# Optimization experiments

Hardware: AMD Instinct MI355X
Metric: run time of the kernel (lower is better)

## Reference

```python
import jax, jax.numpy as jnp
import numpy as np
import math

B, S, D, H = 2, 2048, 1024, 16
HD = D // H  # head_dim = 64
ROPE_BASE = 100000
EPS = 1e-09


def _linear_init(key, in_f, out_f):
    std = min(1.0, math.sqrt(out_f / in_f)) / math.sqrt(in_f)
    return jax.random.normal(key, (in_f, out_f)) * std


def setup_inputs() -> dict:
    key = jax.random.key(0)
    ks = jax.random.split(key, 7)
    Q = jax.random.normal(ks[0], (B, S, D), dtype=jnp.float32)
    K = jax.random.normal(ks[1], (B, S, D), dtype=jnp.float32)
    V = jax.random.normal(ks[2], (B, S, D), dtype=jnp.float32)
    mask = jnp.tril(jnp.ones((S, S), dtype=bool))  # causal
    Wq = _linear_init(ks[3], D, D)
    Wk = _linear_init(ks[4], D, D)
    Wv = _linear_init(ks[5], D, D)
    Wo = _linear_init(ks[6], D, D)
    return {"Q": Q, "K": K, "V": V, "mask": mask,
            "Wq": Wq, "Wk": Wk, "Wv": Wv, "Wo": Wo}


def _rope_tables(seq_len, d):
    positions = jnp.arange(0, seq_len)
    freqs = ROPE_BASE ** (jnp.arange(0, d, 2) / d)
    gamma = positions[:, None] * (1.0 / freqs)[None, :]  # [t, d/2]
    return jnp.cos(gamma).astype(jnp.bfloat16), jnp.sin(gamma).astype(jnp.bfloat16)


def _apply_rope(x, cos, sin):
    # x: [..., t, d]; cos/sin: [t, d/2]
    d = x.shape[-1]
    x1, x2 = x[..., : d // 2], x[..., d // 2:]
    y1 = x1 * cos + x2 * sin
    y2 = -x1 * sin + x2 * cos
    return jnp.concatenate([y1, y2], axis=-1)


def _rms_norm(x):
    rms = jnp.sqrt(jnp.mean(jnp.square(x), axis=-1, keepdims=True) + EPS)
    return x / rms


def reference(Q, K, V, mask, Wq, Wk, Wv, Wo):
    cos, sin = _rope_tables(S, HD)
    q = jnp.dot(Q, Wq)
    k = jnp.dot(K, Wk)
    v = jnp.dot(V, Wv)
    # [B, S, D] -> [B, H, S, HD]
    split = lambda t: t.reshape(*t.shape[:-1], H, HD).swapaxes(-3, -2)
    q, k, v = split(q), split(k), split(v)
    q = _rms_norm(_apply_rope(q, cos, sin))
    k = _rms_norm(_apply_rope(k, cos, sin))
    logits = jnp.einsum('bhqd,bhkd->bhqk', q, k) / jnp.sqrt(jnp.float32(HD))
    logits = jnp.where(mask[None, None, :, :], logits, -1000000000.0)
    attn = jax.nn.softmax(logits, axis=-1)
    vals = jnp.einsum('bhqk,bhkd->bhqd', attn, v)
    # [B, H, S, HD] -> [B, S, D]
    vals = vals.swapaxes(-3, -2).reshape(B, S, D)
    return jnp.dot(vals, Wo)
```

## Files before the change

kernel.cpp:

```cpp
#include <hip/hip_runtime.h>
#include <hip/hip_bf16.h>
#include <stdint.h>

typedef __hip_bfloat16 bf16;
typedef __attribute__((ext_vector_type(8))) short short8;
typedef __attribute__((ext_vector_type(4))) short short4v;
typedef __attribute__((ext_vector_type(4))) float float4v;

static constexpr int nB = 2, nS = 2048, nD = 1024, nH = 16, nHD = 64;
static constexpr int nBS = nB * nS;

#define AS_GLOBAL __attribute__((address_space(1)))
#define AS_LDS    __attribute__((address_space(3)))

union Frag16B { short8 v; uint4 u4; uint2 u2[2]; };

__device__ __forceinline__ void gload_lds16(const void* g, void* l) {
  __builtin_amdgcn_global_load_lds((AS_GLOBAL uint32_t*)(g), (AS_LDS uint32_t*)(l), 16, 0, 0);
}

__device__ __forceinline__ float fast_exp2(float x) {
#if __has_builtin(__builtin_amdgcn_exp2f)
  return __builtin_amdgcn_exp2f(x);
#else
  float r; asm volatile("v_exp_f32 %0, %1" : "=v"(r) : "v"(x)); return r;
#endif
}

__device__ __forceinline__ void lds_barrier() {
  asm volatile("s_waitcnt lgkmcnt(0)\ns_barrier" ::: "memory");
}

__device__ __forceinline__ void lgkm_wait() {
  asm volatile("s_waitcnt lgkmcnt(0)" ::: "memory");
}

__global__ __launch_bounds__(256) void prep_kernel(
    const float* __restrict__ Qin, const float* __restrict__ Kin, const float* __restrict__ Vin,
    const float* __restrict__ Wq, const float* __restrict__ Wk,
    const float* __restrict__ Wv, const float* __restrict__ Wo,
    bf16* __restrict__ Qbf, bf16* __restrict__ Kbf, bf16* __restrict__ Vbf,
    bf16* __restrict__ WqT, bf16* __restrict__ WkT, bf16* __restrict__ WvT, bf16* __restrict__ WoT,
    bf16* __restrict__ cos_t, bf16* __restrict__ sin_t) {
  __shared__ float tile[64][65];
  int bx = blockIdx.x, t = threadIdx.x;
  if (bx < 3072) {
    int tz = bx >> 10, blk = bx & 1023;
    const float* src = tz == 0 ? Qin : tz == 1 ? Kin : Vin;
    bf16* dst = tz == 0 ? Qbf : tz == 1 ? Kbf : Vbf;
#pragma unroll
    for (int i = 0; i < 4; ++i) {
      int idx = blk * 1024 + i * 256 + t;
      float4 v = ((const float4*)src)[idx];
      union { bf16 b[4]; uint2 u; } tmp;
      tmp.b[0] = __float2bfloat16(v.x);
      tmp.b[1] = __float2bfloat16(v.y);
      tmp.b[2] = __float2bfloat16(v.z);
      tmp.b[3] = __float2bfloat16(v.w);
      ((uint2*)dst)[idx] = tmp.u;
    }
  } else if (bx < 4096) {
    int idx = bx - 3072;
    int z = idx >> 8;
    const float* W = z == 0 ? Wq : z == 1 ? Wk : z == 2 ? Wv : Wo;
    bf16* T = z == 0 ? WqT : z == 1 ? WkT : z == 2 ? WvT : WoT;
    int tk = (idx & 15) * 64, tn = ((idx >> 4) & 15) * 64;
    int c = t & 63, r0 = t >> 6;
#pragma unroll
    for (int i = 0; i < 16; ++i) {
      int r = i * 4 + r0;
      tile[r][c] = W[(size_t)(tk + r) * nD + tn + c];
    }
    __syncthreads();
#pragma unroll
    for (int i = 0; i < 16; ++i) {
      int r = i * 4 + r0;
      T[(size_t)(tn + r) * nD + tk + c] = __float2bfloat16(tile[c][r]);
    }
  } else {
    int base = (bx - 4096) * 1024 + t * 4;
#pragma unroll
    for (int i = 0; i < 4; ++i) {
      int e = base + i;
      int s = e >> 5, j = e & 31;
      float inv_freq = powf(100000.0f, -(float)(2 * j) / 64.0f);
      float g = (float)s * inv_freq;
      cos_t[e] = __float2bfloat16(cosf(g));
      sin_t[e] = __float2bfloat16(sinf(g));
    }
  }
}

__global__ __launch_bounds__(256, 3) void gemm_qkv_kernel(
    const bf16* __restrict__ A0, const bf16* __restrict__ A1, const bf16* __restrict__ A2,
    const bf16* __restrict__ Bt0, const bf16* __restrict__ Bt1, const bf16* __restrict__ Bt2,
    bf16* __restrict__ q_h, bf16* __restrict__ k_h, bf16* __restrict__ vt_h,
    const bf16* __restrict__ cos_t, const bf16* __restrict__ sin_t) {
  const int bid = blockIdx.x;
  const int swz = (bid & 7) * 96 + (bid >> 3);
  const int z = swz >> 8;
  const int rem = swz & 255;
  const int n0 = (rem >> 5) * 128;
  const int m0 = (rem & 31) * 128;

  const bf16* __restrict__ A  = z == 0 ? A0 : (z == 1 ? A1 : A2);
  const bf16* __restrict__ Bt = z == 0 ? Bt0 : (z == 1 ? Bt1 : Bt2);

  __shared__ bf16 As[2 * 128 * 32];
  __shared__ bf16 Bs[2 * 128 * 32];

  const int t = threadIdx.x;
  const int lane = t & 63;
  const int wid = t >> 6;
  const int quad = lane >> 4;
  const int l16 = lane & 15;
  const int wm = wid >> 1;
  const int wn = wid & 1;

  const int sc    = (t & 7) ^ ((t >> 3) & 7);
  const int sml   = 2 * (t >> 3) + (sc >> 2);
  const int skoff = (sc & 3) * 8;
  const int swave = wid * 512;

  const int R0a = wm * 32 + (l16 >> 1);
  const int R0b = wn * 32 + (l16 >> 1);
  const int cpar = (l16 & 1) * 4;
  const int abase = R0a * 64 + (((cpar + quad) ^ (R0a & 7)) * 8);
  const int bbase = R0b * 64 + (((cpar + quad) ^ (R0b & 7)) * 8);

#define STAGE_A(KT, BUF) do { \
    const bf16* ag_ = A + (size_t)(m0 + sml) * nD + (KT) * 32 + skoff; \
    gload_lds16(ag_, As + (BUF) + swave); \
    gload_lds16(ag_ + (size_t)64 * nD, As + (BUF) + 2048 + swave); \
  } while (0)
#define STAGE_B(KT, BUF) do { \
    const bf16* bg_ = Bt + (size_t)(n0 + sml) * nD + (KT) * 32 + skoff; \
    gload_lds16(bg_, Bs + (BUF) + swave); \
    gload_lds16(bg_ + (size_t)64 * nD, Bs + (BUF) + 2048 + swave); \
  } while (0)

  float4v acc[4][4] = {};

  STAGE_A(0, 0);
  STAGE_B(0, 0);
  STAGE_A(1, 4096);
  asm volatile("s_waitcnt vmcnt(2)" ::: "memory");
  __builtin_amdgcn_s_barrier();

#pragma unroll 2
  for (int T = 0; T < 32; ++T) {
    const int cu = (T & 1) * 4096;
    const int nx = cu ^ 4096;

    if (T < 31) STAGE_B(T + 1, nx);
    Frag16B fa[4], fb[4];
#pragma unroll
    for (int mi = 0; mi < 4; ++mi) fa[mi].u4 = *(const uint4*)&As[cu + abase + mi * 512];
#pragma unroll
    for (int ni = 0; ni < 4; ++ni) fb[ni].u4 = *(const uint4*)&Bs[cu + bbase + ni * 512];
    __builtin_amdgcn_s_setprio(1);
#pragma unroll
    for (int mi = 0; mi < 2; ++mi)
#pragma unroll
      for (int ni = 0; ni < 4; ++ni)
        acc[mi][ni] = __builtin_amdgcn_mfma_f32_16x16x32_bf16(fa[mi].v, fb[ni].v, acc[mi][ni], 0, 0, 0);
    __builtin_amdgcn_s_setprio(0);
    __builtin_amdgcn_s_barrier();

    asm volatile("s_waitcnt lgkmcnt(0)" ::: "memory");
    __builtin_amdgcn_s_setprio(1);
#pragma unroll
    for (int ni = 0; ni < 4; ++ni)
      acc[2][ni] = __builtin_amdgcn_mfma_f32_16x16x32_bf16(fa[2].v, fb[ni].v, acc[2][ni], 0, 0, 0);
    __builtin_amdgcn_s_setprio(0);
    __builtin_amdgcn_s_barrier();

    if (T < 30) STAGE_A(T + 2, cu);
    __builtin_amdgcn_s_setprio(1);
#pragma unroll
    for (int ni = 0; ni < 4; ++ni)
      acc[3][ni] = __builtin_amdgcn_mfma_f32_16x16x32_bf16(fa[3].v, fb[ni].v, acc[3][ni], 0, 0, 0);
    __builtin_amdgcn_s_setprio(0);
    if (T < 30) { asm volatile("s_waitcnt vmcnt(2)" ::: "memory"); }
    else        { asm volatile("s_waitcnt vmcnt(0)" ::: "memory"); }
    __builtin_amdgcn_s_barrier();
  }
#undef STAGE_A
#undef STAGE_B

  const int col0 = n0 + wn * 64;
  if (z <= 1) {
    bf16* dst = z ? k_h : q_h;
#pragma unroll
    for (int mi = 0; mi < 4; ++mi)
#pragma unroll
      for (int r = 0; r < 4; ++r) {
        int row = m0 + wm * 64 + mi * 16 + quad * 4 + r;
        int s = row & (nS - 1);
        float x0 = acc[mi][0][r], x1 = acc[mi][1][r], x2 = acc[mi][2][r], x3 = acc[mi][3][r];
        float y[4];
#pragma unroll
        for (int p = 0; p < 2; ++p) {
          int d = p * 16 + l16;
          float c = __bfloat162float(cos_t[s * 32 + d]);
          float sn = __bfloat162float(sin_t[s * 32 + d]);
          float xa = p ? x1 : x0, xb = p ? x3 : x2;
          y[p] = xa * c + xb * sn;
          y[p + 2] = xb * c - xa * sn;
        }
        float ss = y[0] * y[0] + y[1] * y[1] + y[2] * y[2] + y[3] * y[3];
#pragma unroll
        for (int m = 1; m <= 8; m <<= 1) ss += __shfl_xor(ss, m, 64);
        float inv = 1.0f / sqrtf(ss * (1.0f / 64.0f) + 1e-9f);
#pragma unroll
        for (int ni = 0; ni < 4; ++ni)
          dst[(size_t)row * nD + col0 + ni * 16 + l16] = __float2bfloat16(y[ni] * inv);
      }
  } else {
#pragma unroll
    for (int mi = 0; mi < 4; ++mi)
#pragma unroll
      for (int r = 0; r < 4; ++r) {
        int row = m0 + wm * 64 + mi * 16 + quad * 4 + r;
        int b = row >> 11, s = row & (nS - 1);
#pragma unroll
        for (int ni = 0; ni < 4; ++ni) {
          int col = col0 + ni * 16 + l16;
          int h = col >> 6, d = col & 63;
          vt_h[((size_t)((b * nH + h) * 64 + d)) * nS + s] = __float2bfloat16(acc[mi][ni][r]);
        }
      }
  }
}

__global__ __launch_bounds__(256) void gemm_out_kernel(
    const bf16* __restrict__ A, const bf16* __restrict__ Bt, float* __restrict__ C) {
  __shared__ bf16 As[64 * 64];
  __shared__ bf16 Bs[128 * 64];
  const int t = threadIdx.x;
  const int lane = t & 63;
  const int wid = t >> 6;
  const int quad = lane >> 4;
  const int l16 = lane & 15;
  const int wm = wid >> 1;
  const int wn = wid & 1;
  const int m0 = blockIdx.x * 64;
  const int n0 = blockIdx.y * 128;
  const int K = nD;
  const int rloc = lane >> 3, cl = lane & 7;
  const int cg = cl ^ rloc;

  float4v acc[2][4] = {};
  for (int kt = 0; kt < K; kt += 64) {
    __syncthreads();
#pragma unroll
    for (int p = 0; p < 2; ++p) {
      int rowbase = (p * 4 + wid) * 8;
      gload_lds16(A + (size_t)(m0 + rowbase + rloc) * K + kt + cg * 8, As + (size_t)rowbase * 64);
    }
#pragma unroll
    for (int p = 0; p < 4; ++p) {
      int rowbase = (p * 4 + wid) * 8;
      gload_lds16(Bt + (size_t)(n0 + rowbase + rloc) * K + kt + cg * 8, Bs + (size_t)rowbase * 64);
    }
    __syncthreads();

#pragma unroll
    for (int ks = 0; ks < 2; ++ks) {
      Frag16B a[2], b[4];
#pragma unroll
      for (int mi = 0; mi < 2; ++mi) {
        int row = wm * 32 + mi * 16 + l16;
        int ch = (ks * 4 + quad) ^ (row & 7);
        a[mi].u4 = *(const uint4*)&As[row * 64 + ch * 8];
      }
#pragma unroll
      for (int ni = 0; ni < 4; ++ni) {
        int row = wn * 64 + ni * 16 + l16;
        int ch = (ks * 4 + quad) ^ (row & 7);
        b[ni].u4 = *(const uint4*)&Bs[row * 64 + ch * 8];
      }
#pragma unroll
      for (int mi = 0; mi < 2; ++mi)
#pragma unroll
        for (int ni = 0; ni < 4; ++ni)
          acc[mi][ni] = __builtin_amdgcn_mfma_f32_16x16x32_bf16(a[mi].v, b[ni].v, acc[mi][ni], 0, 0, 0);
    }
  }
#pragma unroll
  for (int mi = 0; mi < 2; ++mi)
#pragma unroll
    for (int ni = 0; ni < 4; ++ni)
#pragma unroll
      for (int r = 0; r < 4; ++r) {
        int row = m0 + wm * 32 + mi * 16 + quad * 4 + r;
        int col = n0 + wn * 64 + ni * 16 + l16;
        C[(size_t)row * nD + col] = acc[mi][ni][r];
      }
}

static constexpr float SC = 0.18033688011112042f;

__global__ __launch_bounds__(512, 4) void attn_kernel(const bf16* __restrict__ q_h,
                                                      const bf16* __restrict__ k_h,
                                                      const bf16* __restrict__ vt_h,
                                                      bf16* __restrict__ vals) {
  __shared__ bf16 lds_buf[4 * 8192];

  const int t = threadIdx.x;
  const int lane = t & 63, wid = t >> 6, quad = lane >> 4, l16 = lane & 15;
  const int id = blockIdx.x;
  const int xcd = id & 7;
  const int j = id >> 3;
  const int jj = j & 31;
  const int bh = xcd * 4 + (jj & 3);
  const int u = jj >> 2;
  const int qt = (j < 32) ? (15 - u) : u;
  const int b = bh >> 4, h = bh & 15;

  const bf16* Kbase = k_h + ((size_t)b * nS) * nD + h * 64;
  const bf16* Vbase = vt_h + (size_t)bh * 64 * nS;

  const int rl = lane >> 3;
  const int cg8 = ((lane & 7) ^ rl) * 8;
  const int r7 = l16 & 7;

  bf16* const scratch = lds_buf + wid * 1152;

  const int q0w = qt * 128 + wid * 16;

  Frag16B qf[2];
  {
    const bf16* qp = q_h + ((size_t)(b * nS + q0w + l16)) * nD + h * 64;
    qf[0].u4 = *(const uint4*)(qp + quad * 8);
    qf[1].u4 = *(const uint4*)(qp + 32 + quad * 8);
  }

#define STAGE_KV(KT) do { \
    const int bo_ = ((KT) & 1) * 8192; \
    const bf16* kg_ = Kbase + (size_t)((KT) * 128 + wid * 16 + rl) * nD + cg8; \
    gload_lds16(kg_, lds_buf + bo_ + wid * 1024); \
    gload_lds16(kg_ + (size_t)8 * nD, lds_buf + bo_ + wid * 1024 + 512); \
    const bf16* vg_ = Vbase + (size_t)(wid * 8 + rl) * nS + (KT) * 128 + cg8; \
    gload_lds16(vg_, lds_buf + 16384 + bo_ + wid * 512); \
    gload_lds16(vg_ + 64, lds_buf + 16384 + bo_ + 4096 + wid * 512); \
  } while (0)

#define QKH(Kb, HB, ST) do { \
    _Pragma("unroll") \
    for (int kt4 = 0; kt4 < 4; ++kt4) { \
      int row = (HB) * 64 + kt4 * 16 + l16; \
      Frag16B k0_, k1_; \
      k0_.u4 = *(const uint4*)&(Kb)[row * 64 + ((quad ^ r7) * 8)]; \
      k1_.u4 = *(const uint4*)&(Kb)[row * 64 + (((quad + 4) ^ r7) * 8)]; \
      float4v zz_ = {}; \
      zz_ = __builtin_amdgcn_mfma_f32_16x16x32_bf16(k0_.v, qf[0].v, zz_, 0, 0, 0); \
      (ST)[kt4] = __builtin_amdgcn_mfma_f32_16x16x32_bf16(k1_.v, qf[1].v, zz_, 0, 0, 0); \
    } \
  } while (0)

#define EXPH(ST, PF) do { \
    _Pragma("unroll") \
    for (int kt4 = 0; kt4 < 4; ++kt4) \
      _Pragma("unroll") \
      for (int r = 0; r < 4; ++r) { \
        float p_ = fast_exp2((ST)[kt4][r] * SC); \
        l_acc += p_; \
        union { bf16 hh; short ss; } cv_; \
        cv_.hh = __float2bfloat16(p_); \
        (PF)[kt4][r] = cv_.ss; \
      } \
  } while (0)

#define EXPHM(ST, PF, HB) do { \
    int qg_ = q0w + l16; \
    _Pragma("unroll") \
    for (int kt4 = 0; kt4 < 4; ++kt4) { \
      int key0_ = qt * 128 + (HB) * 64 + kt4 * 16 + quad * 4; \
      _Pragma("unroll") \
      for (int r = 0; r < 4; ++r) { \
        float x_ = (ST)[kt4][r] * SC; \
        if (key0_ + r > qg_) x_ = -12000.0f; \
        float p_ = fast_exp2(x_); \
        l_acc += p_; \
        union { bf16 hh; short ss; } cv_; \
        cv_.hh = __float2bfloat16(p_); \
        (PF)[kt4][r] = cv_.ss; \
      } \
    } \
  } while (0)

#define PVH(Vb, HB, PF) do { \
    _Pragma("unroll") \
    for (int dt = 0; dt < 4; ++dt) { \
      int row = dt * 16 + l16; \
      _Pragma("unroll") \
      for (int kt4 = 0; kt4 < 4; ++kt4) { \
        int chunk_ = kt4 * 2 + (quad >> 1); \
        union { uint2 u; short4v s; } vv_; \
        vv_.u = *(const uint2*)&(Vb)[(HB) * 4096 + row * 64 + ((chunk_ ^ r7) * 8) + (quad & 1) * 4]; \
        o_acc[dt] = __builtin_amdgcn_mfma_f32_16x16x16bf16_1k(vv_.s, (PF)[kt4], o_acc[dt], 0, 0, 0); \
      } \
    } \
  } while (0)

  STAGE_KV(0);
  asm volatile("s_waitcnt vmcnt(0)" ::: "memory");
  __builtin_amdgcn_s_barrier();

  float4v o_acc[4] = {};
  float l_acc = 0.f;

  for (int kt = 0; kt < qt; ++kt) {
    STAGE_KV(kt + 1);
    const bf16* Kb = lds_buf + (kt & 1) * 8192;
    const bf16* Vb = lds_buf + 16384 + (kt & 1) * 8192;

    float4v st0[4], st1[4];
    __builtin_amdgcn_s_setprio(1);
    QKH(Kb, 0, st0);
    QKH(Kb, 1, st1);
    __builtin_amdgcn_s_setprio(0);

    short4v pf[4];
    EXPH(st0, pf);
    __builtin_amdgcn_s_setprio(1);
    PVH(Vb, 0, pf);
    __builtin_amdgcn_s_setprio(0);
    EXPH(st1, pf);
    __builtin_amdgcn_s_setprio(1);
    PVH(Vb, 1, pf);
    __builtin_amdgcn_s_setprio(0);

    asm volatile("s_waitcnt vmcnt(0) lgkmcnt(0)" ::: "memory");
    __builtin_amdgcn_s_barrier();
  }

  {
    const bf16* Kb = lds_buf + (qt & 1) * 8192;
    const bf16* Vb = lds_buf + 16384 + (qt & 1) * 8192;

    float4v st0[4];
    QKH(Kb, 0, st0);
    short4v pf[4];
    EXPHM(st0, pf, 0);
    PVH(Vb, 0, pf);

    if (wid >= 4) {
      float4v st1[4];
      QKH(Kb, 1, st1);
      EXPHM(st1, pf, 1);
      PVH(Vb, 1, pf);
    }
  }
#undef STAGE_KV
#undef QKH
#undef EXPH
#undef EXPHM
#undef PVH

  lds_barrier();

  float la = l_acc;
  la += __shfl_xor(la, 16, 64);
  la += __shfl_xor(la, 32, 64);
  float inv_l = 1.0f / la;
#pragma unroll
  for (int dt = 0; dt < 4; ++dt) {
    union { bf16 b2[2]; uint u; } p01, p23;
    p01.b2[0] = __float2bfloat16(o_acc[dt][0] * inv_l);
    p01.b2[1] = __float2bfloat16(o_acc[dt][1] * inv_l);
    p23.b2[0] = __float2bfloat16(o_acc[dt][2] * inv_l);
    p23.b2[1] = __float2bfloat16(o_acc[dt][3] * inv_l);
    *(uint*)&scratch[l16 * 72 + dt * 16 + quad * 4] = p01.u;
    *(uint*)&scratch[l16 * 72 + dt * 16 + quad * 4 + 2] = p23.u;
  }
  lgkm_wait();
  uint4 r0 = *(const uint4*)&scratch[l16 * 72 + quad * 16];
  uint4 r1 = *(const uint4*)&scratch[l16 * 72 + quad * 16 + 8];
  int qrow = q0w + l16;
  bf16* vp = vals + ((size_t)(b * nS + qrow)) * nD + h * 64 + quad * 16;
  *(uint4*)(vp) = r0;
  *(uint4*)(vp + 8) = r1;
}

extern "C" void kernel_launch(void* const* d_in, const int* in_sizes, int n_in,
                              void* d_out, int out_size, void* d_ws, size_t ws_size,
                              hipStream_t stream) {
  const float* Qin = (const float*)d_in[0];
  const float* Kin = (const float*)d_in[1];
  const float* Vin = (const float*)d_in[2];
  const float* Wq = (const float*)d_in[4];
  const float* Wk = (const float*)d_in[5];
  const float* Wv = (const float*)d_in[6];
  const float* Wo = (const float*)d_in[7];
  float* out = (float*)d_out;

  char* ws = (char*)d_ws;
  const size_t MB = 1u << 20;
  bf16* Qbf = (bf16*)(ws + 0 * MB);
  bf16* Kbf = (bf16*)(ws + 8 * MB);
  bf16* Vbf = (bf16*)(ws + 16 * MB);
  bf16* WqT = (bf16*)(ws + 24 * MB);
  bf16* WkT = (bf16*)(ws + 26 * MB);
  bf16* WvT = (bf16*)(ws + 28 * MB);
  bf16* WoT = (bf16*)(ws + 30 * MB);
  bf16* cos_t = (bf16*)(ws + 32 * MB);
  bf16* sin_t = (bf16*)(ws + 33 * MB);
  bf16* q_h = (bf16*)(ws + 34 * MB);
  bf16* k_h = (bf16*)(ws + 42 * MB);
  bf16* vt_h = (bf16*)(ws + 50 * MB);
  bf16* vals = (bf16*)(ws + 58 * MB);

  prep_kernel<<<4160, 256, 0, stream>>>(Qin, Kin, Vin, Wq, Wk, Wv, Wo,
                                        Qbf, Kbf, Vbf, WqT, WkT, WvT, WoT, cos_t, sin_t);

  gemm_qkv_kernel<<<768, 256, 0, stream>>>(Qbf, Kbf, Vbf, WqT, WkT, WvT,
                                           q_h, k_h, vt_h, cos_t, sin_t);

  attn_kernel<<<512, 512, 0, stream>>>(q_h, k_h, vt_h, vals);

  gemm_out_kernel<<<dim3(64, 8), 256, 0, stream>>>(vals, WoT, out);
}
```

Baseline: 208.9 us.

## Widen GEMM K-tiles to 64 and double-buffer out-projection GEMM

The QKV GEMM now stages 64-wide K tiles (16 iterations instead of 32) into a single double-buffered pipeline with one barrier per iteration, in place of the finer interleaved schedule. Occupancy drops from 3 to 2 blocks because LDS use doubles. The output GEMM gains double buffering with prefetch of the next tile, a 1D grid with n-fastest block ordering, and the same 64-wide swizzled fragment loads. The aim is fewer barriers and better load/compute overlap. The cost is more LDS per block, lower occupancy, and a coarser pipeline where the MFMAs no longer interleave with the waits.

```diff
diff --git a/kernel.cpp b/kernel.cpp
--- a/kernel.cpp
+++ b/kernel.cpp
@@ -91,7 +91,7 @@
   }
 }
 
-__global__ __launch_bounds__(256, 3) void gemm_qkv_kernel(
+__global__ __launch_bounds__(256, 2) void gemm_qkv_kernel(
     const bf16* __restrict__ A0, const bf16* __restrict__ A1, const bf16* __restrict__ A2,
     const bf16* __restrict__ Bt0, const bf16* __restrict__ Bt1, const bf16* __restrict__ Bt2,
     bf16* __restrict__ q_h, bf16* __restrict__ k_h, bf16* __restrict__ vt_h,
@@ -106,87 +106,78 @@
   const bf16* __restrict__ A  = z == 0 ? A0 : (z == 1 ? A1 : A2);
   const bf16* __restrict__ Bt = z == 0 ? Bt0 : (z == 1 ? Bt1 : Bt2);
 
-  __shared__ bf16 As[2 * 128 * 32];
-  __shared__ bf16 Bs[2 * 128 * 32];
+  __shared__ bf16 As[2 * 128 * 64];
+  __shared__ bf16 Bs[2 * 128 * 64];
 
   const int t = threadIdx.x;
   const int lane = t & 63;
   const int wid = t >> 6;
   const int quad = lane >> 4;
   const int l16 = lane & 15;
+  const int r7 = l16 & 7;
   const int wm = wid >> 1;
   const int wn = wid & 1;
 
-  const int sc    = (t & 7) ^ ((t >> 3) & 7);
-  const int sml   = 2 * (t >> 3) + (sc >> 2);
-  const int skoff = (sc & 3) * 8;
-  const int swave = wid * 512;
-
-  const int R0a = wm * 32 + (l16 >> 1);
-  const int R0b = wn * 32 + (l16 >> 1);
-  const int cpar = (l16 & 1) * 4;
-  const int abase = R0a * 64 + (((cpar + quad) ^ (R0a & 7)) * 8);
-  const int bbase = R0b * 64 + (((cpar + quad) ^ (R0b & 7)) * 8);
-
-#define STAGE_A(KT, BUF) do { \
-    const bf16* ag_ = A + (size_t)(m0 + sml) * nD + (KT) * 32 + skoff; \
-    gload_lds16(ag_, As + (BUF) + swave); \
-    gload_lds16(ag_ + (size_t)64 * nD, As + (BUF) + 2048 + swave); \
-  } while (0)
-#define STAGE_B(KT, BUF) do { \
-    const bf16* bg_ = Bt + (size_t)(n0 + sml) * nD + (KT) * 32 + skoff; \
-    gload_lds16(bg_, Bs + (BUF) + swave); \
-    gload_lds16(bg_ + (size_t)64 * nD, Bs + (BUF) + 2048 + swave); \
+  const int srow = t >> 3;
+  const int scg8 = ((t & 7) ^ (srow & 7)) * 8;
+
+  const int ch0 = (quad ^ r7) * 8;
+  const int ch1 = ch0 ^ 32;
+  const int arow = (wm * 64 + l16) * 64;
+  const int brow = (wn * 64 + l16) * 64;
+
+#define STAGE(KT, BUF) do { \
+    const bf16* ag_ = A + (size_t)(m0 + srow) * nD + (KT) * 64 + scg8; \
+    const bf16* bg_ = Bt + (size_t)(n0 + srow) * nD + (KT) * 64 + scg8; \
+    _Pragma("unroll") \
+    for (int i = 0; i < 4; ++i) { \
+      gload_lds16(ag_ + (size_t)(i * 32) * nD, As + (BUF) + i * 2048 + wid * 512); \
+      gload_lds16(bg_ + (size_t)(i * 32) * nD, Bs + (BUF) + i * 2048 + wid * 512); \
+    } \
   } while (0)
 
   float4v acc[4][4] = {};
 
-  STAGE_A(0, 0);
-  STAGE_B(0, 0);
-  STAGE_A(1, 4096);
-  asm volatile("s_waitcnt vmcnt(2)" ::: "memory");
+  STAGE(0, 0);
+  asm volatile("s_waitcnt vmcnt(0)" ::: "memory");
   __builtin_amdgcn_s_barrier();
 
 #pragma unroll 2
-  for (int T = 0; T < 32; ++T) {
-    const int cu = (T & 1) * 4096;
-    const int nx = cu ^ 4096;
-
-    if (T < 31) STAGE_B(T + 1, nx);
-    Frag16B fa[4], fb[4];
-#pragma unroll
-    for (int mi = 0; mi < 4; ++mi) fa[mi].u4 = *(const uint4*)&As[cu + abase + mi * 512];
-#pragma unroll
-    for (int ni = 0; ni < 4; ++ni) fb[ni].u4 = *(const uint4*)&Bs[cu + bbase + ni * 512];
+  for (int T = 0; T < 16; ++T) {
+    const int cu = (T & 1) * 8192;
+    const int nx = cu ^ 8192;
+
+    if (T < 15) STAGE(T + 1, nx);
+
+    Frag16B fa0[4], fa1[4], fb0[4], fb1[4];
+#pragma unroll
+    for (int mi = 0; mi < 4; ++mi) {
+      fa0[mi].u4 = *(const uint4*)&As[cu + arow + mi * 1024 + ch0];
+      fa1[mi].u4 = *(const uint4*)&As[cu + arow + mi * 1024 + ch1];
+    }
+#pragma unroll
+    for (int ni = 0; ni < 4; ++ni) {
+      fb0[ni].u4 = *(const uint4*)&Bs[cu + brow + ni * 1024 + ch0];
+      fb1[ni].u4 = *(const uint4*)&Bs[cu + brow + ni * 1024 + ch1];
+    }
+
     __builtin_amdgcn_s_setprio(1);
 #pragma unroll
-    for (int mi = 0; mi < 2; ++mi)
+    for (int mi = 0; mi < 4; ++mi)
 #pragma unroll
       for (int ni = 0; ni < 4; ++ni)
-        acc[mi][ni] = __builtin_amdgcn_mfma_f32_16x16x32_bf16(fa[mi].v, fb[ni].v, acc[mi][ni], 0, 0, 0);
+        acc[mi][ni] = __builtin_amdgcn_mfma_f32_16x16x32_bf16(fa0[mi].v, fb0[ni].v, acc[mi][ni], 0, 0, 0);
+#pragma unroll
+    for (int mi = 0; mi < 4; ++mi)
+#pragma unroll
+      for (int ni = 0; ni < 4; ++ni)
+        acc[mi][ni] = __builtin_amdgcn_mfma_f32_16x16x32_bf16(fa1[mi].v, fb1[ni].v, acc[mi][ni], 0, 0, 0);
     __builtin_amdgcn_s_setprio(0);
+
+    asm volatile("s_waitcnt vmcnt(0)" ::: "memory");
     __builtin_amdgcn_s_barrier();
-
-    asm volatile("s_waitcnt lgkmcnt(0)" ::: "memory");
-    __builtin_amdgcn_s_setprio(1);
-#pragma unroll
-    for (int ni = 0; ni < 4; ++ni)
-      acc[2][ni] = __builtin_amdgcn_mfma_f32_16x16x32_bf16(fa[2].v, fb[ni].v, acc[2][ni], 0, 0, 0);
-    __builtin_amdgcn_s_setprio(0);
-    __builtin_amdgcn_s_barrier();
-
-    if (T < 30) STAGE_A(T + 2, cu);
-    __builtin_amdgcn_s_setprio(1);
-#pragma unroll
-    for (int ni = 0; ni < 4; ++ni)
-      acc[3][ni] = __builtin_amdgcn_mfma_f32_16x16x32_bf16(fa[3].v, fb[ni].v, acc[3][ni], 0, 0, 0);
-    __builtin_amdgcn_s_setprio(0);
-    if (T < 30) { asm volatile("s_waitcnt vmcnt(2)" ::: "memory"); }
-    else        { asm volatile("s_waitcnt vmcnt(0)" ::: "memory"); }
-    __builtin_amdgcn_s_barrier();
-  }
-#undef STAGE_A
-#undef STAGE_B
+  }
+#undef STAGE
 
   const int col0 = n0 + wn * 64;
   if (z <= 1) {
@@ -233,60 +224,83 @@
   }
 }
 
-__global__ __launch_bounds__(256) void gemm_out_kernel(
+__global__ __launch_bounds__(256, 2) void gemm_out_kernel(
     const bf16* __restrict__ A, const bf16* __restrict__ Bt, float* __restrict__ C) {
-  __shared__ bf16 As[64 * 64];
-  __shared__ bf16 Bs[128 * 64];
+  __shared__ bf16 As[2 * 64 * 64];
+  __shared__ bf16 Bs[2 * 128 * 64];
+  const int bid = blockIdx.x;
+  const int n0 = (bid & 7) * 128;
+  const int m0 = (bid >> 3) * 64;
   const int t = threadIdx.x;
   const int lane = t & 63;
   const int wid = t >> 6;
   const int quad = lane >> 4;
   const int l16 = lane & 15;
+  const int r7 = l16 & 7;
   const int wm = wid >> 1;
   const int wn = wid & 1;
-  const int m0 = blockIdx.x * 64;
-  const int n0 = blockIdx.y * 128;
-  const int K = nD;
-  const int rloc = lane >> 3, cl = lane & 7;
-  const int cg = cl ^ rloc;
+
+  const int srow = t >> 3;
+  const int scg8 = ((t & 7) ^ (srow & 7)) * 8;
+
+  const int ch0 = (quad ^ r7) * 8;
+  const int ch1 = ch0 ^ 32;
+  const int arow = (wm * 32 + l16) * 64;
+  const int brow = (wn * 64 + l16) * 64;
+
+#define STAGE_O(KT, AB, BB) do { \
+    const bf16* ag_ = A + (size_t)(m0 + srow) * nD + (KT) * 64 + scg8; \
+    const bf16* bg_ = Bt + (size_t)(n0 + srow) * nD + (KT) * 64 + scg8; \
+    gload_lds16(ag_, As + (AB) + wid * 512); \
+    gload_lds16(ag_ + (size_t)32 * nD, As + (AB) + 2048 + wid * 512); \
+    _Pragma("unroll") \
+    for (int i = 0; i < 4; ++i) \
+      gload_lds16(bg_ + (size_t)(i * 32) * nD, Bs + (BB) + i * 2048 + wid * 512); \
+  } while (0)
 
   float4v acc[2][4] = {};
-  for (int kt = 0; kt < K; kt += 64) {
-    __syncthreads();
-#pragma unroll
-    for (int p = 0; p < 2; ++p) {
-      int rowbase = (p * 4 + wid) * 8;
-      gload_lds16(A + (size_t)(m0 + rowbase + rloc) * K + kt + cg * 8, As + (size_t)rowbase * 64);
-    }
-#pragma unroll
-    for (int p = 0; p < 4; ++p) {
-      int rowbase = (p * 4 + wid) * 8;
-      gload_lds16(Bt + (size_t)(n0 + rowbase + rloc) * K + kt + cg * 8, Bs + (size_t)rowbase * 64);
-    }
-    __syncthreads();
-
-#pragma unroll
-    for (int ks = 0; ks < 2; ++ks) {
-      Frag16B a[2], b[4];
-#pragma unroll
-      for (int mi = 0; mi < 2; ++mi) {
-        int row = wm * 32 + mi * 16 + l16;
-        int ch = (ks * 4 + quad) ^ (row & 7);
-        a[mi].u4 = *(const uint4*)&As[row * 64 + ch * 8];
-      }
-#pragma unroll
-      for (int ni = 0; ni < 4; ++ni) {
-        int row = wn * 64 + ni * 16 + l16;
-        int ch = (ks * 4 + quad) ^ (row & 7);
-        b[ni].u4 = *(const uint4*)&Bs[row * 64 + ch * 8];
-      }
-#pragma unroll
-      for (int mi = 0; mi < 2; ++mi)
-#pragma unroll
-        for (int ni = 0; ni < 4; ++ni)
-          acc[mi][ni] = __builtin_amdgcn_mfma_f32_16x16x32_bf16(a[mi].v, b[ni].v, acc[mi][ni], 0, 0, 0);
-    }
-  }
+
+  STAGE_O(0, 0, 0);
+  asm volatile("s_waitcnt vmcnt(0)" ::: "memory");
+  __builtin_amdgcn_s_barrier();
+
+#pragma unroll 2
+  for (int T = 0; T < 16; ++T) {
+    const int cua = (T & 1) * 4096;
+    const int cub = (T & 1) * 8192;
+
+    if (T < 15) STAGE_O(T + 1, cua ^ 4096, cub ^ 8192);
+
+    Frag16B a0[2], a1[2], b0[4], b1[4];
+#pragma unroll
+    for (int mi = 0; mi < 2; ++mi) {
+      a0[mi].u4 = *(const uint4*)&As[cua + arow + mi * 1024 + ch0];
+      a1[mi].u4 = *(const uint4*)&As[cua + arow + mi * 1024 + ch1];
+    }
+#pragma unroll
+    for (int ni = 0; ni < 4; ++ni) {
+      b0[ni].u4 = *(const uint4*)&Bs[cub + brow + ni * 1024 + ch0];
+      b1[ni].u4 = *(const uint4*)&Bs[cub + brow + ni * 1024 + ch1];
+    }
+
+    __builtin_amdgcn_s_setprio(1);
+#pragma unroll
+    for (int mi = 0; mi < 2; ++mi)
+#pragma unroll
+      for (int ni = 0; ni < 4; ++ni)
+        acc[mi][ni] = __builtin_amdgcn_mfma_f32_16x16x32_bf16(a0[mi].v, b0[ni].v, acc[mi][ni], 0, 0, 0);
+#pragma unroll
+    for (int mi = 0; mi < 2; ++mi)
+#pragma unroll
+      for (int ni = 0; ni < 4; ++ni)
+        acc[mi][ni] = __builtin_amdgcn_mfma_f32_16x16x32_bf16(a1[mi].v, b1[ni].v, acc[mi][ni], 0, 0, 0);
+    __builtin_amdgcn_s_setprio(0);
+
+    asm volatile("s_waitcnt vmcnt(0)" ::: "memory");
+    __builtin_amdgcn_s_barrier();
+  }
+#undef STAGE_O
+
 #pragma unroll
   for (int mi = 0; mi < 2; ++mi)
 #pragma unroll
@@ -520,5 +534,5 @@
 
   attn_kernel<<<512, 512, 0, stream>>>(q_h, k_h, vt_h, vals);
 
-  gemm_out_kernel<<<dim3(64, 8), 256, 0, stream>>>(vals, WoT, out);
-}
+  gemm_out_kernel<<<512, 256, 0, stream>>>(vals, WoT, out);
+}
```

Result: slower. 216.6 us (+3.7%).
